# Kernel tuning notes

Hardware: AMD Instinct MI355X
Metric: run time of the kernel (lower is better)

## Reference

```python
import jax, jax.numpy as jnp
import numpy as np

FEATURE_DIM, HIDDEN_DIM, ATTN_DIM = 2048, 1024, 1024
B, L = 128, 196


def setup_inputs() -> dict:
    key = jax.random.key(0)
    ks = jax.random.split(key, 8)
    s_enc = 1.0 / np.sqrt(FEATURE_DIM)
    s_hid = 1.0 / np.sqrt(HIDDEN_DIM)
    s_full = 1.0 / np.sqrt(ATTN_DIM)
    return {
        "encoder_out": jax.random.normal(ks[0], (B, L, FEATURE_DIM), jnp.float32),
        "hidden": jax.random.normal(ks[1], (B, HIDDEN_DIM), jnp.float32),
        "W_enc": jax.random.uniform(ks[2], (FEATURE_DIM, ATTN_DIM), jnp.float32, -s_enc, s_enc),
        "b_enc": jax.random.uniform(ks[3], (ATTN_DIM,), jnp.float32, -s_enc, s_enc),
        "W_hid": jax.random.uniform(ks[4], (HIDDEN_DIM, ATTN_DIM), jnp.float32, -s_hid, s_hid),
        "b_hid": jax.random.uniform(ks[5], (ATTN_DIM,), jnp.float32, -s_hid, s_hid),
        "W_full": jax.random.uniform(ks[6], (ATTN_DIM,), jnp.float32, -s_full, s_full),
        "b_full": jax.random.uniform(ks[7], (1,), jnp.float32, -s_full, s_full),
    }


def reference(encoder_out, hidden, W_enc, b_enc, W_hid, b_hid, W_full, b_full):
    # attn1: (B, L, A)
    attn1 = jnp.einsum("blf,fa->bla", encoder_out, W_enc) + b_enc
    # attn2: (B, 1, A)
    attn2 = (hidden @ W_hid + b_hid)[:, None, :]
    attn = jax.nn.relu(attn1 + attn2)
    # scalar score per location: (B, L)
    scores = jnp.einsum("bla,a->bl", attn, W_full) + b_full[0]
    alpha = jax.nn.softmax(scores, axis=1)
    # weighted sum over L: (B, F)
    context = jnp.einsum("blf,bl->bf", encoder_out, alpha)
    return context, alpha
```

## Files before the change

### kernel.cpp

```cpp
#include <hip/hip_runtime.h>
#include <hip/hip_bf16.h>

typedef unsigned short u16;
typedef short s16x8 __attribute__((ext_vector_type(8)));
typedef unsigned int u32x2 __attribute__((ext_vector_type(2)));
typedef float f32x4 __attribute__((ext_vector_type(4)));

#define F_DIM 2048
#define A_DIM 1024
#define H_DIM 1024
#define BATCH 128
#define LLEN  196
#define MROWS (BATCH * LLEN)
#define MTILES (MROWS / 256)

__device__ __forceinline__ u16 f2b(float x) {
  union { float f; unsigned int u; } c; c.f = x;
  unsigned int r = (c.u + 0x7fffu + ((c.u >> 16) & 1u)) >> 16;
  return (u16)r;
}

__device__ __forceinline__ unsigned int f2b_pk(float a, float b) {
  unsigned int r;
  asm volatile("v_cvt_pk_bf16_f32 %0, %1, %2" : "=v"(r) : "v"(a), "v"(b));
  return r;
}

__device__ __forceinline__ void gload_lds16(const void* g, void* l) {
  __builtin_amdgcn_global_load_lds((const __attribute__((address_space(1))) void*)g,
                                   (__attribute__((address_space(3))) void*)l, 16, 0, 0);
}

__global__ void wenc_cvt_kernel(const float* __restrict__ W, u16* __restrict__ WT) {
  __shared__ float tile[32][33];
  int kb = blockIdx.x * 32, ab = blockIdx.y * 32;
  int t = threadIdx.x;
  int r = t >> 3, c = (t & 7) * 4;
  float4 v = *(const float4*)&W[(size_t)(kb + r) * A_DIM + ab + c];
  tile[r][c] = v.x; tile[r][c + 1] = v.y; tile[r][c + 2] = v.z; tile[r][c + 3] = v.w;
  __syncthreads();
  ushort4 o;
  o.x = f2b(tile[c + 0][r]);
  o.y = f2b(tile[c + 1][r]);
  o.z = f2b(tile[c + 2][r]);
  o.w = f2b(tile[c + 3][r]);
  *(ushort4*)&WT[(size_t)(ab + r) * F_DIM + kb + c] = o;
}

__global__ __launch_bounds__(256) void attn2_kernel(
    const float* __restrict__ hidden, const float* __restrict__ W_hid,
    const float* __restrict__ b_hid, const float* __restrict__ b_enc,
    float* __restrict__ attn2p) {
  __shared__ float hl[4][H_DIM];
  int t = threadIdx.x;
  int a  = blockIdx.x * 256 + t;
  int b0 = blockIdx.y * 4;
  float* hf = &hl[0][0];
  #pragma unroll
  for (int j = 0; j < 4; ++j) {
    int s = j * 256 + t;
    *(float4*)&hf[s * 4] = *(const float4*)&hidden[(size_t)b0 * H_DIM + s * 4];
  }
  __syncthreads();
  float acc[4] = {0.f, 0.f, 0.f, 0.f};
  #pragma unroll 4
  for (int k = 0; k < H_DIM; ++k) {
    float w = W_hid[(size_t)k * A_DIM + a];
    #pragma unroll
    for (int j = 0; j < 4; ++j) acc[j] = fmaf(hl[j][k], w, acc[j]);
  }
  float bias = b_hid[a] + b_enc[a];
  #pragma unroll
  for (int j = 0; j < 4; ++j)
    attn2p[(size_t)(b0 + j) * A_DIM + a] = acc[j] + bias;
}

__global__ __launch_bounds__(512, 2) void gemm_score(
    const float* __restrict__ enc, const u16* __restrict__ WT,
    const float* __restrict__ attn2p, const float* __restrict__ W_full,
    float* __restrict__ scores) {
  __shared__ __align__(16) u16 As[2 * 16384];
  __shared__ __align__(16) u16 Bs[2 * 16384];

  int i = blockIdx.x;
  int g = i >> 5, r = i & 31;
  int y = r >> 3, gi = r & 7;
  int mt = g * 8 + gi;
  if (mt >= MTILES) return;
  int m0 = mt * 256, n0 = y * 256;
  int t = threadIdx.x;
  int lane = t & 63, wave = t >> 6;
  int wr = wave >> 2, wc = wave & 3;
  int c16 = lane & 15, quad = lane >> 4;

  const float* aP = enc + (size_t)(m0 + (t >> 2)) * F_DIM + (t & 3) * 4;
  int awo[4];
  #pragma unroll
  for (int s = 0; s < 4; ++s)
    awo[s] = (t >> 2) * 64 + ((t & 3) & 1) * 4
           + (((s * 2 + ((t & 3) >> 1)) ^ ((t >> 2) & 7)) * 8);
  const u16* bgp = WT + (size_t)(n0 + (t >> 3)) * F_DIM + ((t & 7) ^ ((t >> 3) & 7)) * 8;

  const int akey = c16 & 7;
  int gsw[2];
  gsw[0] = ((0 * 4 + quad) ^ akey) * 8;
  gsw[1] = ((1 * 4 + quad) ^ akey) * 8;
  const int aro = (wr * 128 + c16) * 64;
  const int bro = (wc * 64 + c16) * 64;

  f32x4 acc[8][4];
  #pragma unroll
  for (int mi = 0; mi < 8; ++mi)
    #pragma unroll
    for (int ni = 0; ni < 4; ++ni) acc[mi][ni] = (f32x4){0.f, 0.f, 0.f, 0.f};

  s16x8 af[4][2], bf[2][2];
  float4 R0lo[4], R0hi[4], R1lo[4], R1hi[4];

#define ALD(RX, half, kt_) do {                                                 \
    const float* p_ = aP + (size_t)(half) * 128 * F_DIM + (kt_) * 64;           \
    RX[0] = *(const float4*)(p_);                                               \
    RX[1] = *(const float4*)(p_ + 16);                                          \
    RX[2] = *(const float4*)(p_ + 32);                                          \
    RX[3] = *(const float4*)(p_ + 48);                                          \
  } while (0)

#define AWR(RX, cb, half) do {                                                  \
    _Pragma("unroll")                                                           \
    for (int s_ = 0; s_ < 4; ++s_) {                                            \
      u32x2 w_; w_.x = f2b_pk(RX[s_].x, RX[s_].y);                              \
      w_.y = f2b_pk(RX[s_].z, RX[s_].w);                                        \
      *(u32x2*)&As[(cb) * 16384 + (half) * 8192 + awo[s_]] = w_;                \
    }                                                                           \
  } while (0)

#define BGL(cb, kt_) do {                                                       \
    _Pragma("unroll")                                                           \
    for (int s_ = 0; s_ < 4; ++s_)                                              \
      gload_lds16(bgp + (size_t)s_ * 64 * F_DIM + (size_t)(kt_) * 64,           \
                  Bs + (cb) * 16384 + s_ * 4096 + wave * 512);                  \
  } while (0)

#define DSRA(cb, mh)                                                            \
    _Pragma("unroll")                                                           \
    for (int i_ = 0; i_ < 4; ++i_)                                              \
      _Pragma("unroll")                                                         \
      for (int h_ = 0; h_ < 2; ++h_)                                            \
        af[i_][h_] = *(const s16x8*)&As[(cb) * 16384 + aro                      \
                                        + ((mh) * 4 + i_) * 1024 + gsw[h_]];

#define DSRB(cb, nh)                                                            \
    _Pragma("unroll")                                                           \
    for (int j_ = 0; j_ < 2; ++j_)                                              \
      _Pragma("unroll")                                                         \
      for (int h_ = 0; h_ < 2; ++h_)                                            \
        bf[j_][h_] = *(const s16x8*)&Bs[(cb) * 16384 + bro                      \
                                        + ((nh) * 2 + j_) * 1024 + gsw[h_]];

#define PHTAIL(mh, nh) do {                                                     \
    __builtin_amdgcn_s_barrier();                                               \
    asm volatile("s_waitcnt lgkmcnt(0)" ::: "memory");                          \
    __builtin_amdgcn_s_setprio(1);                                              \
    _Pragma("unroll")                                                           \
    for (int i_ = 0; i_ < 4; ++i_)                                              \
      _Pragma("unroll")                                                         \
      for (int j_ = 0; j_ < 2; ++j_)                                            \
        _Pragma("unroll")                                                       \
        for (int h_ = 0; h_ < 2; ++h_)                                          \
          acc[(mh) * 4 + i_][(nh) * 2 + j_] =                                   \
              __builtin_amdgcn_mfma_f32_16x16x32_bf16(                          \
                  af[i_][h_], bf[j_][h_],                                       \
                  acc[(mh) * 4 + i_][(nh) * 2 + j_], 0, 0, 0);                  \
    __builtin_amdgcn_s_setprio(0);                                              \
    __builtin_amdgcn_s_barrier();                                               \
  } while (0)

#define GROUP(T_, RB_, WB_, WLO_, WHI_, LLO_, LHI_) do {                        \
    int kB_ = min((T_) + 1, 31);                                                \
    int kA_ = min((T_) + 2, 31);                                                \
                                                                        \
    DSRA(RB_, 0); DSRB(RB_, 0);                                                 \
    AWR(WLO_, WB_, 0);                                                          \
    BGL(WB_, kB_);                                                              \
    PHTAIL(0, 0);                                                               \
                                                                        \
    DSRB(RB_, 1);                                                               \
    AWR(WHI_, WB_, 1);                                                          \
    ALD(LLO_, 0, kA_);                                                          \
    PHTAIL(0, 1);                                                               \
                                                                        \
    DSRA(RB_, 1); DSRB(RB_, 0);                                                 \
    ALD(LHI_, 1, kA_);                                                          \
    PHTAIL(1, 0);                                                               \
                                                                        \
    DSRB(RB_, 1);                                                               \
    asm volatile("s_waitcnt vmcnt(8)" ::: "memory");                            \
    PHTAIL(1, 1);                                                               \
  } while (0)

  ALD(R0lo, 0, 0);
  ALD(R0hi, 1, 0);
  BGL(0, 0);
  asm volatile("s_waitcnt vmcnt(4)" ::: "memory");
  AWR(R0lo, 0, 0);
  AWR(R0hi, 0, 1);
  ALD(R1lo, 0, 1);
  ALD(R1hi, 1, 1);
  asm volatile("s_waitcnt vmcnt(8) lgkmcnt(0)" ::: "memory");
  __builtin_amdgcn_s_barrier();

  #pragma unroll 1
  for (int T = 0; T < 32; T += 2) {
    GROUP(T,     0, 1, R1lo, R1hi, R0lo, R0hi);
    GROUP(T + 1, 1, 0, R0lo, R0hi, R1lo, R1hi);
  }
#undef GROUP
#undef PHTAIL
#undef DSRA
#undef DSRB
#undef BGL
#undef AWR
#undef ALD

  int bfirst = m0 / LLEN;
  int bnd1 = (bfirst + 1) * LLEN, bnd2 = (bfirst + 2) * LLEN;
  int b1c = min(bfirst + 1, BATCH - 1), b2c = min(bfirst + 2, BATCH - 1);
  float wf[4], a2v0[4], a2v1[4], a2v2[4];
  #pragma unroll
  for (int ni = 0; ni < 4; ++ni) {
    int col = n0 + wc * 64 + ni * 16 + c16;
    wf[ni]   = W_full[col];
    a2v0[ni] = attn2p[(size_t)bfirst * A_DIM + col];
    a2v1[ni] = attn2p[(size_t)b1c * A_DIM + col];
    a2v2[ni] = attn2p[(size_t)b2c * A_DIM + col];
  }
  #pragma unroll
  for (int mi = 0; mi < 8; ++mi) {
    #pragma unroll
    for (int rr = 0; rr < 4; ++rr) {
      int row_g = m0 + wr * 128 + mi * 16 + quad * 4 + rr;
      float p = 0.f;
      #pragma unroll
      for (int ni = 0; ni < 4; ++ni) {
        float a2 = row_g >= bnd1 ? (row_g >= bnd2 ? a2v2[ni] : a2v1[ni]) : a2v0[ni];
        float v = acc[mi][ni][rr] + a2;
        v = fmaxf(v, 0.f);
        p = fmaf(v, wf[ni], p);
      }
      p += __shfl_xor(p, 1);
      p += __shfl_xor(p, 2);
      p += __shfl_xor(p, 4);
      p += __shfl_xor(p, 8);
      if (c16 == 0) atomicAdd(&scores[row_g], p);
    }
  }
}

__global__ void softmax_kernel(const float* __restrict__ scores, float* __restrict__ alpha) {
  __shared__ float red[8];
  int b = blockIdx.x, t = threadIdx.x;
  float s = (t < LLEN) ? scores[b * LLEN + t] : -3.0e38f;
  float m = s;
  #pragma unroll
  for (int o = 1; o <= 32; o <<= 1) m = fmaxf(m, __shfl_xor(m, o));
  if ((t & 63) == 0) red[t >> 6] = m;
  __syncthreads();
  m = fmaxf(fmaxf(red[0], red[1]), fmaxf(red[2], red[3]));
  float e = (t < LLEN) ? expf(s - m) : 0.f;
  float sum = e;
  #pragma unroll
  for (int o = 1; o <= 32; o <<= 1) sum += __shfl_xor(sum, o);
  __syncthreads();
  if ((t & 63) == 0) red[4 + (t >> 6)] = sum;
  __syncthreads();
  sum = red[4] + red[5] + red[6] + red[7];
  if (t < LLEN) alpha[b * LLEN + t] = e / sum;
}

__global__ __launch_bounds__(256) void context_kernel(
    const float* __restrict__ enc, const float* __restrict__ alpha,
    float* __restrict__ out) {
  __shared__ float al[LLEN];
  __shared__ float4 part[4][64];
  int b = blockIdx.y, t = threadIdx.x;
  if (t < LLEN) al[t] = alpha[b * LLEN + t];
  __syncthreads();
  int f4 = blockIdx.x * 64 + (t & 63);
  int lq = t >> 6;
  const float4* e4 = (const float4*)enc
                   + ((size_t)b * LLEN + lq * 49) * (F_DIM / 4) + f4;
  float4 acc = {0.f, 0.f, 0.f, 0.f};
  #pragma unroll 7
  for (int j = 0; j < 49; ++j) {
    float4 v = e4[(size_t)j * (F_DIM / 4)];
    float a = al[lq * 49 + j];
    acc.x = fmaf(v.x, a, acc.x);
    acc.y = fmaf(v.y, a, acc.y);
    acc.z = fmaf(v.z, a, acc.z);
    acc.w = fmaf(v.w, a, acc.w);
  }
  part[lq][t & 63] = acc;
  __syncthreads();
  if (t < 64) {
    float4 p0 = part[0][t], p1 = part[1][t], p2 = part[2][t], p3 = part[3][t];
    float4 s;
    s.x = (p0.x + p1.x) + (p2.x + p3.x);
    s.y = (p0.y + p1.y) + (p2.y + p3.y);
    s.z = (p0.z + p1.z) + (p2.z + p3.z);
    s.w = (p0.w + p1.w) + (p2.w + p3.w);
    *(float4*)(out + (size_t)b * F_DIM + (size_t)(blockIdx.x * 64 + t) * 4) = s;
  }
}

extern "C" void kernel_launch(void* const* d_in, const int* in_sizes, int n_in,
                              void* d_out, int out_size, void* d_ws, size_t ws_size,
                              hipStream_t stream) {
  const float* enc    = (const float*)d_in[0];
  const float* hidden = (const float*)d_in[1];
  const float* W_enc  = (const float*)d_in[2];
  const float* b_enc  = (const float*)d_in[3];
  const float* W_hid  = (const float*)d_in[4];
  const float* b_hid  = (const float*)d_in[5];
  const float* W_full = (const float*)d_in[6];
  float* out = (float*)d_out;
  float* alpha_out = out + (size_t)BATCH * F_DIM;

  const size_t wt_bytes = (size_t)A_DIM * F_DIM * sizeof(u16);
  const size_t a2_bytes = (size_t)BATCH * A_DIM * sizeof(float);
  const size_t sc_bytes = (size_t)MROWS * sizeof(float);
  char* ws = (char*)d_ws;
  u16*   WT     = (u16*)ws;
  float* attn2p = (float*)(ws + wt_bytes);
  float* scores = (float*)(ws + wt_bytes + a2_bytes);

  hipMemsetAsync(scores, 0, sc_bytes, stream);

  wenc_cvt_kernel<<<dim3(F_DIM / 32, A_DIM / 32), 256, 0, stream>>>(W_enc, WT);
  attn2_kernel<<<dim3(A_DIM / 256, BATCH / 4), 256, 0, stream>>>(hidden, W_hid, b_hid, b_enc, attn2p);
  gemm_score<<<dim3(416), 512, 0, stream>>>(enc, WT, attn2p, W_full, scores);
  softmax_kernel<<<dim3(BATCH), 256, 0, stream>>>(scores, alpha_out);
  context_kernel<<<dim3(8, BATCH), 256, 0, stream>>>(enc, alpha_out, out);
}
```

Before: 550.9 us.

## Merge prep kernels, split-K attn2, fuse softmax into context, reorder GEMM loads

The weight conversion and the hidden projection now run as one launch. The hidden projection is split along K into 8 chunks of 128 and accumulated with atomics into a buffer that is zeroed together with the scores. The softmax is fused into the context kernel: every block recomputes the softmax of its row, and only the first block writes alpha. Inside the GEMM group macro the global A loads are issued earlier and the LDS writes later, giving more time to hide load latency. The cost is more atomics and softmax work repeated 8 times per row, and the atomic accumulation makes the summation order nondeterministic.

```diff
diff --git a/kernel.cpp b/kernel.cpp
--- a/kernel.cpp
+++ b/kernel.cpp
@@ -31,48 +31,53 @@
                                    (__attribute__((address_space(3))) void*)l, 16, 0, 0);
 }
 
-__global__ void wenc_cvt_kernel(const float* __restrict__ W, u16* __restrict__ WT) {
-  __shared__ float tile[32][33];
-  int kb = blockIdx.x * 32, ab = blockIdx.y * 32;
-  int t = threadIdx.x;
-  int r = t >> 3, c = (t & 7) * 4;
-  float4 v = *(const float4*)&W[(size_t)(kb + r) * A_DIM + ab + c];
-  tile[r][c] = v.x; tile[r][c + 1] = v.y; tile[r][c + 2] = v.z; tile[r][c + 3] = v.w;
-  __syncthreads();
-  ushort4 o;
-  o.x = f2b(tile[c + 0][r]);
-  o.y = f2b(tile[c + 1][r]);
-  o.z = f2b(tile[c + 2][r]);
-  o.w = f2b(tile[c + 3][r]);
-  *(ushort4*)&WT[(size_t)(ab + r) * F_DIM + kb + c] = o;
-}
-
-__global__ __launch_bounds__(256) void attn2_kernel(
+__global__ __launch_bounds__(256) void prep_kernel(
+    const float* __restrict__ W, u16* __restrict__ WT,
     const float* __restrict__ hidden, const float* __restrict__ W_hid,
     const float* __restrict__ b_hid, const float* __restrict__ b_enc,
     float* __restrict__ attn2p) {
-  __shared__ float hl[4][H_DIM];
   int t = threadIdx.x;
-  int a  = blockIdx.x * 256 + t;
-  int b0 = blockIdx.y * 4;
-  float* hf = &hl[0][0];
-  #pragma unroll
-  for (int j = 0; j < 4; ++j) {
-    int s = j * 256 + t;
-    *(float4*)&hf[s * 4] = *(const float4*)&hidden[(size_t)b0 * H_DIM + s * 4];
-  }
-  __syncthreads();
-  float acc[4] = {0.f, 0.f, 0.f, 0.f};
-  #pragma unroll 4
-  for (int k = 0; k < H_DIM; ++k) {
-    float w = W_hid[(size_t)k * A_DIM + a];
+  if (blockIdx.x < 2048) {
+    __shared__ float tile[32][33];
+    int id = blockIdx.x;
+    int kb = (id & 63) * 32, ab = (id >> 6) * 32;
+    int r = t >> 3, c = (t & 7) * 4;
+    float4 v = *(const float4*)&W[(size_t)(kb + r) * A_DIM + ab + c];
+    tile[r][c] = v.x; tile[r][c + 1] = v.y; tile[r][c + 2] = v.z; tile[r][c + 3] = v.w;
+    __syncthreads();
+    ushort4 o;
+    o.x = f2b(tile[c + 0][r]);
+    o.y = f2b(tile[c + 1][r]);
+    o.z = f2b(tile[c + 2][r]);
+    o.w = f2b(tile[c + 3][r]);
+    *(ushort4*)&WT[(size_t)(ab + r) * F_DIM + kb + c] = o;
+  } else {
+    __shared__ float hl[8][128];
+    int id = blockIdx.x - 2048;
+    int a  = (id & 3) * 256 + t;
+    int b0 = ((id >> 2) & 15) * 8;
+    int k0 = (id >> 6) * 128;
+    {
+      int j = t >> 5, kk = (t & 31) * 4;
+      float4 v = *(const float4*)&hidden[(size_t)(b0 + j) * H_DIM + k0 + kk];
+      hl[j][kk + 0] = v.x; hl[j][kk + 1] = v.y; hl[j][kk + 2] = v.z; hl[j][kk + 3] = v.w;
+    }
+    __syncthreads();
+    float acc[8] = {0.f, 0.f, 0.f, 0.f, 0.f, 0.f, 0.f, 0.f};
+    #pragma unroll 4
+    for (int k = 0; k < 128; ++k) {
+      float w = W_hid[(size_t)(k0 + k) * A_DIM + a];
+      #pragma unroll
+      for (int j = 0; j < 8; ++j) acc[j] = fmaf(hl[j][k], w, acc[j]);
+    }
+    if ((id >> 6) == 0) {
+      float bias = b_hid[a] + b_enc[a];
+      #pragma unroll
+      for (int j = 0; j < 8; ++j) acc[j] += bias;
+    }
     #pragma unroll
-    for (int j = 0; j < 4; ++j) acc[j] = fmaf(hl[j][k], w, acc[j]);
-  }
-  float bias = b_hid[a] + b_enc[a];
-  #pragma unroll
-  for (int j = 0; j < 4; ++j)
-    attn2p[(size_t)(b0 + j) * A_DIM + a] = acc[j] + bias;
+    for (int j = 0; j < 8; ++j) atomicAdd(&attn2p[(size_t)(b0 + j) * A_DIM + a], acc[j]);
+  }
 }
 
 __global__ __launch_bounds__(512, 2) void gemm_score(
@@ -180,17 +185,17 @@
     int kA_ = min((T_) + 2, 31);                                                \
                                                                         \
     DSRA(RB_, 0); DSRB(RB_, 0);                                                 \
-    AWR(WLO_, WB_, 0);                                                          \
     BGL(WB_, kB_);                                                              \
+    ALD(LLO_, 0, kA_);                                                          \
     PHTAIL(0, 0);                                                               \
                                                                         \
     DSRB(RB_, 1);                                                               \
-    AWR(WHI_, WB_, 1);                                                          \
-    ALD(LLO_, 0, kA_);                                                          \
+    ALD(LHI_, 1, kA_);                                                          \
+    AWR(WLO_, WB_, 0);                                                          \
     PHTAIL(0, 1);                                                               \
                                                                         \
     DSRA(RB_, 1); DSRB(RB_, 0);                                                 \
-    ALD(LHI_, 1, kA_);                                                          \
+    AWR(WHI_, WB_, 1);                                                          \
     PHTAIL(1, 0);                                                               \
                                                                         \
     DSRB(RB_, 1);                                                               \
@@ -256,9 +261,13 @@
   }
 }
 
-__global__ void softmax_kernel(const float* __restrict__ scores, float* __restrict__ alpha) {
+__global__ __launch_bounds__(256) void context_kernel(
+    const float* __restrict__ enc, const float* __restrict__ scores,
+    float* __restrict__ alpha_out, float* __restrict__ out) {
+  __shared__ float al[LLEN];
   __shared__ float red[8];
-  int b = blockIdx.x, t = threadIdx.x;
+  __shared__ float4 part[4][64];
+  int b = blockIdx.y, t = threadIdx.x;
   float s = (t < LLEN) ? scores[b * LLEN + t] : -3.0e38f;
   float m = s;
   #pragma unroll
@@ -270,20 +279,14 @@
   float sum = e;
   #pragma unroll
   for (int o = 1; o <= 32; o <<= 1) sum += __shfl_xor(sum, o);
-  __syncthreads();
   if ((t & 63) == 0) red[4 + (t >> 6)] = sum;
   __syncthreads();
   sum = red[4] + red[5] + red[6] + red[7];
-  if (t < LLEN) alpha[b * LLEN + t] = e / sum;
-}
-
-__global__ __launch_bounds__(256) void context_kernel(
-    const float* __restrict__ enc, const float* __restrict__ alpha,
-    float* __restrict__ out) {
-  __shared__ float al[LLEN];
-  __shared__ float4 part[4][64];
-  int b = blockIdx.y, t = threadIdx.x;
-  if (t < LLEN) al[t] = alpha[b * LLEN + t];
+  float av = e / sum;
+  if (t < LLEN) {
+    al[t] = av;
+    if (blockIdx.x == 0) alpha_out[b * LLEN + t] = av;
+  }
   __syncthreads();
   int f4 = blockIdx.x * 64 + (t & 63);
   int lq = t >> 6;
@@ -303,12 +306,12 @@
   __syncthreads();
   if (t < 64) {
     float4 p0 = part[0][t], p1 = part[1][t], p2 = part[2][t], p3 = part[3][t];
-    float4 s;
-    s.x = (p0.x + p1.x) + (p2.x + p3.x);
-    s.y = (p0.y + p1.y) + (p2.y + p3.y);
-    s.z = (p0.z + p1.z) + (p2.z + p3.z);
-    s.w = (p0.w + p1.w) + (p2.w + p3.w);
-    *(float4*)(out + (size_t)b * F_DIM + (size_t)(blockIdx.x * 64 + t) * 4) = s;
+    float4 sv;
+    sv.x = (p0.x + p1.x) + (p2.x + p3.x);
+    sv.y = (p0.y + p1.y) + (p2.y + p3.y);
+    sv.z = (p0.z + p1.z) + (p2.z + p3.z);
+    sv.w = (p0.w + p1.w) + (p2.w + p3.w);
+    *(float4*)(out + (size_t)b * F_DIM + (size_t)(blockIdx.x * 64 + t) * 4) = sv;
   }
 }
 
@@ -333,11 +336,9 @@
   float* attn2p = (float*)(ws + wt_bytes);
   float* scores = (float*)(ws + wt_bytes + a2_bytes);
 
-  hipMemsetAsync(scores, 0, sc_bytes, stream);
-
-  wenc_cvt_kernel<<<dim3(F_DIM / 32, A_DIM / 32), 256, 0, stream>>>(W_enc, WT);
-  attn2_kernel<<<dim3(A_DIM / 256, BATCH / 4), 256, 0, stream>>>(hidden, W_hid, b_hid, b_enc, attn2p);
+  hipMemsetAsync(attn2p, 0, a2_bytes + sc_bytes, stream);
+
+  prep_kernel<<<dim3(2048 + 512), 256, 0, stream>>>(W_enc, WT, hidden, W_hid, b_hid, b_enc, attn2p);
   gemm_score<<<dim3(416), 512, 0, stream>>>(enc, WT, attn2p, W_full, scores);
-  softmax_kernel<<<dim3(BATCH), 256, 0, stream>>>(scores, alpha_out);
-  context_kernel<<<dim3(8, BATCH), 256, 0, stream>>>(enc, alpha_out, out);
-}
+  context_kernel<<<dim3(8, BATCH), 256, 0, stream>>>(enc, scores, alpha_out, out);
+}
```

Measured after the change: 503.6 us. 8.6% less time.
